# Kernel optimization log

Measured on AMD Instinct MI355X. Metric: run time of the kernel, lower is better.

## Reference

```python
import jax, jax.numpy as jnp
import numpy as np

N_POINTS = 500_000
NUM_SUPERNODES = 8192
MAX_DEGREE = 32
HIDDEN = 192
NDIM = 3
INPUT_DIM = 3
MAX_WAVELENGTH = 10000.0


def setup_inputs() -> dict:
    key = jax.random.key(0)
    k = jax.random.split(key, 8)
    rng = np.random.default_rng(0)
    # supernodes: unique node indices; each supernode gets MAX_DEGREE neighbor edges
    supernode_idx = np.sort(rng.choice(N_POINTS, size=NUM_SUPERNODES, replace=False))
    dst_idx = np.repeat(supernode_idx, MAX_DEGREE)              # [E] destination node ids
    src_idx = rng.integers(0, N_POINTS, size=NUM_SUPERNODES * MAX_DEGREE)  # [E] source node ids
    return {
        "input_feat": jax.random.normal(k[0], (N_POINTS, INPUT_DIM), dtype=jnp.float32),
        "input_pos": jax.random.uniform(k[1], (N_POINTS, NDIM), dtype=jnp.float32),
        "src_idx": jnp.asarray(src_idx, dtype=jnp.int64 if jax.config.jax_enable_x64 else jnp.int32),
        "dst_idx": jnp.asarray(dst_idx, dtype=jnp.int64 if jax.config.jax_enable_x64 else jnp.int32),
        "W_in": jax.random.normal(k[2], (INPUT_DIM, HIDDEN), dtype=jnp.float32) * 0.05,
        "b_in": jnp.zeros((HIDDEN,), dtype=jnp.float32),
        "W1": jax.random.normal(k[3], (2 * HIDDEN, HIDDEN), dtype=jnp.float32) * 0.05,
        "b1": jnp.zeros((HIDDEN,), dtype=jnp.float32),
        "W2": jax.random.normal(k[4], (HIDDEN, HIDDEN), dtype=jnp.float32) * 0.05,
        "b2": jnp.zeros((HIDDEN,), dtype=jnp.float32),
    }


def _sincos_embed(pos):
    # ContinuousSincosEmbed: HIDDEN split across NDIM axes, sin/cos halves each
    dim_per_axis = HIDDEN // NDIM  # 64 (even -> no padding)
    omega = 1.0 / MAX_WAVELENGTH ** (
        jnp.arange(0, dim_per_axis, 2, dtype=jnp.float32) / dim_per_axis
    )  # [32]
    ang = pos[:, :, None] * omega  # [N, NDIM, 32]
    emb = jnp.concatenate([jnp.sin(ang), jnp.cos(ang)], axis=-1)  # [N, NDIM, 64]
    return emb.reshape(pos.shape[0], HIDDEN)


def reference(input_feat, input_pos, src_idx, dst_idx, W_in, b_in, W1, b1, W2, b2):
    # node embedding: input projection + continuous sincos positional embed
    x = jnp.dot(input_feat, W_in) + b_in + _sincos_embed(input_pos)  # [N, H]
    # gather + concat edge features: [E, 2H]
    msg = jnp.concatenate([x[src_idx], x[dst_idx]], axis=1)
    # 2-layer message MLP (Linear-GELU-Linear)
    h = jax.nn.gelu(jnp.dot(msg, W1) + b1, approximate=False)
    h = jnp.dot(h, W2) + b2  # [E, H]
    # segment-mean over destination supernodes (fixed degree -> uniform counts)
    E = src_idx.shape[0]
    S = E // MAX_DEGREE
    seg = jnp.repeat(jnp.arange(S), MAX_DEGREE)
    pooled = jax.ops.segment_sum(h, seg, num_segments=S) / MAX_DEGREE  # [S, H]
    return pooled[None]  # [batch_size=1, S, H]
```

## Files before the change

kernel.cpp:

```cpp
#include <hip/hip_runtime.h>

#define DEG 32
#define SAW 232

typedef _Float16 half8 __attribute__((ext_vector_type(8)));
typedef __fp16 fp16x2 __attribute__((ext_vector_type(2)));
typedef float f32x4 __attribute__((ext_vector_type(4)));
typedef int int4v __attribute__((ext_vector_type(4)));

#define EXP2F(x)   __builtin_amdgcn_exp2f(x)
#define SIN_REV(x) __builtin_amdgcn_sinf(x)
#define COS_REV(x) __builtin_amdgcn_cosf(x)
#define RCPF(x)    __builtin_amdgcn_rcpf(x)
#define INV_2PI    0.15915494309189535f
#define TWO_LOG2E  2.8853900817779268f
#define NEG_L2_10K_O32 -0.41524101186092046f

__device__ __forceinline__ float gelu_f(float x){
  float z = 0.7978845608028654f * (x + 0.044715f * x * x * x);
  float e = EXP2F(TWO_LOG2E * z);
  float th = 1.0f - 2.0f * RCPF(1.0f + e);
  return 0.5f * x * (1.0f + th);
}

__device__ __forceinline__ int pkh(float a, float b){
  fp16x2 p = __builtin_amdgcn_cvt_pkrtz(a, b);
  return __builtin_bit_cast(int, p);
}

__device__ __forceinline__ void build_tile(_Float16 (*sA)[SAW], float (*sPos)[3],
    float* sOmg, const int* __restrict__ idx, int idx_stride, int base,
    const float* __restrict__ feat, const float* __restrict__ pos, int t){
  if (t < 32) sOmg[t] = EXP2F((float)t * NEG_L2_10K_O32) * INV_2PI;
  if (t < 64){
    int node = idx[(base + t) * idx_stride];
    sPos[t][0] = pos[3*node]; sPos[t][1] = pos[3*node+1]; sPos[t][2] = pos[3*node+2];
  }
  if (t >= 192){
    int e = t - 192;
    int node = idx[(base + e) * idx_stride];
    float f0 = feat[3*node], f1 = feat[3*node+1], f2 = feat[3*node+2];
    int4v v0; v0[0] = pkh(f0, f1); v0[1] = pkh(f2, 0.f); v0[2] = 0; v0[3] = 0;
    int4v z; z[0] = 0; z[1] = 0; z[2] = 0; z[3] = 0;
    *reinterpret_cast<int4v*>(&sA[e][192]) = v0;
    *reinterpret_cast<int4v*>(&sA[e][200]) = z;
    *reinterpret_cast<int4v*>(&sA[e][208]) = z;
    *reinterpret_cast<int4v*>(&sA[e][216]) = z;
  }
  __syncthreads();
  if (t < 192){
    int lane = t & 63, w = t >> 6;
    int r16 = lane & 15, g = lane >> 4;
    float om[8];
    #pragma unroll
    for (int j = 0; j < 8; j++) om[j] = sOmg[8*g + j];
    #pragma unroll
    for (int rr = 0; rr < 4; rr++){
      int row = r16 + rr*16;
      float p = sPos[row][w];
      float a[8];
      #pragma unroll
      for (int j = 0; j < 8; j++) a[j] = p * om[j];
      int4v sv, cv;
      #pragma unroll
      for (int j = 0; j < 4; j++){
        sv[j] = pkh(SIN_REV(a[2*j]), SIN_REV(a[2*j+1]));
        cv[j] = pkh(COS_REV(a[2*j]), COS_REV(a[2*j+1]));
      }
      int ch = w*8 + g;
      *reinterpret_cast<int4v*>(&sA[row][8*ch])     = sv;
      *reinterpret_cast<int4v*>(&sA[row][8*(ch+4)]) = cv;
    }
  }
  __syncthreads();
}

__device__ __forceinline__ void gemm_tile(f32x4 acc[4][3], const _Float16 (*sA)[SAW],
    const _Float16* __restrict__ Bt, int ln15, int grp, int wave){
  #pragma unroll
  for (int k6 = 0; k6 < 7; k6++){
    half8 Af[4];
    #pragma unroll
    for (int m = 0; m < 4; m++)
      Af[m] = *reinterpret_cast<const half8*>(&sA[m*16 + ln15][k6*32 + grp*8]);
    #pragma unroll
    for (int n = 0; n < 3; n++){
      half8 Bf = *reinterpret_cast<const half8*>(Bt + (wave*48 + n*16 + ln15)*224 + k6*32 + grp*8);
      #pragma unroll
      for (int m = 0; m < 4; m++)
        acc[m][n] = __builtin_amdgcn_mfma_f32_16x16x32_f16(Af[m], Bf, acc[m][n], 0, 0, 0);
    }
  }
}

__global__ void k0_prep(const float* __restrict__ W_in, const float* __restrict__ b_in,
    const float* __restrict__ W1, const float* __restrict__ b1,
    const float* __restrict__ W2,
    _Float16* __restrict__ w1tc, _Float16* __restrict__ w1bc,
    _Float16* __restrict__ w2t, float* __restrict__ bias_c){
  int id = blockIdx.x * 256 + threadIdx.x;
  if (id < 86016){
    int half_sel = id / 43008;
    int i = id - half_sel * 43008;
    int n = i / 224, k = i - n * 224;
    const float* Wh = W1 + half_sel * 192 * 192;
    _Float16* dst = half_sel ? w1bc : w1tc;
    if (k < 192) dst[i] = (_Float16)Wh[k*192 + n];
    else if (k < 195){
      int r = k - 192;
      float s = 0.f;
      for (int m = 0; m < 192; m++) s += W_in[r*192 + m] * Wh[m*192 + n];
      dst[i] = (_Float16)s;
    } else dst[i] = (_Float16)0.f;
  } else if (id < 122880){
    int i = id - 86016;
    int n = i / 192, k = i - n * 192;
    w2t[i] = (_Float16)(W2[k*192 + n] * 0.03125f);
  } else if (id < 123072){
    int n = id - 122880;
    float s = b1[n];
    for (int m = 0; m < 192; m++) s += b_in[m] * (W1[m*192 + n] + W1[(192+m)*192 + n]);
    bias_c[n] = s;
  }
}

__global__ __launch_bounds__(256) void k1_dst(const int* __restrict__ dst_idx,
    const float* __restrict__ feat, const float* __restrict__ pos,
    const _Float16* __restrict__ w1bc, const float* __restrict__ bias_c,
    _Float16* __restrict__ a_dst){
  __shared__ _Float16 sA[64][SAW];
  __shared__ float sPos[64][3];
  __shared__ float sOmg[32];
  int blk = blockIdx.x, t = threadIdx.x;
  build_tile(sA, sPos, sOmg, dst_idx, DEG, blk*64, feat, pos, t);
  int wave = t >> 6, lane = t & 63, ln15 = lane & 15, grp = lane >> 4;
  f32x4 acc[4][3];
  #pragma unroll
  for (int m = 0; m < 4; m++)
    #pragma unroll
    for (int n = 0; n < 3; n++) acc[m][n] = (f32x4){0.f, 0.f, 0.f, 0.f};
  gemm_tile(acc, sA, w1bc, ln15, grp, wave);
  #pragma unroll
  for (int n = 0; n < 3; n++){
    int col = wave*48 + n*16 + ln15;
    float bias = bias_c[col];
    #pragma unroll
    for (int m = 0; m < 4; m++)
      #pragma unroll
      for (int r = 0; r < 4; r++)
        a_dst[(blk*64 + m*16 + grp*4 + r)*192 + col] = (_Float16)(acc[m][n][r] + bias);
  }
}

__global__ __launch_bounds__(256) void k2_edge(const int* __restrict__ src_idx,
    const float* __restrict__ feat, const float* __restrict__ pos,
    const _Float16* __restrict__ w1tc, const _Float16* __restrict__ a_dst,
    _Float16* __restrict__ S1){
  __shared__ _Float16 sA[64][SAW];
  __shared__ float sPos[64][3];
  __shared__ float sOmg[32];
  int blk = blockIdx.x, t = threadIdx.x;
  build_tile(sA, sPos, sOmg, src_idx, 1, blk*64, feat, pos, t);
  int wave = t >> 6, lane = t & 63, ln15 = lane & 15, grp = lane >> 4;
  f32x4 acc[4][3];
  #pragma unroll
  for (int m = 0; m < 4; m++)
    #pragma unroll
    for (int n = 0; n < 3; n++) acc[m][n] = (f32x4){0.f, 0.f, 0.f, 0.f};
  gemm_tile(acc, sA, w1tc, ln15, grp, wave);
  const _Float16* adp = a_dst + blk*2*192;
  #pragma unroll
  for (int h = 0; h < 2; h++){
    #pragma unroll
    for (int n = 0; n < 3; n++){
      int col = wave*48 + n*16 + ln15;
      float ad = (float)adp[h*192 + col];
      float cs = 0.f;
      #pragma unroll
      for (int mm = 0; mm < 2; mm++){
        f32x4 a = acc[h*2 + mm][n];
        #pragma unroll
        for (int r = 0; r < 4; r++) cs += gelu_f(a[r] + ad);
      }
      cs += __shfl_xor(cs, 16, 64);
      cs += __shfl_xor(cs, 32, 64);
      if (grp == 0)
        S1[(blk*2 + h)*192 + col] = (_Float16)cs;
    }
  }
}

__global__ __launch_bounds__(256) void k3_out(const _Float16* __restrict__ S1,
    const _Float16* __restrict__ w2t, const float* __restrict__ b2,
    float* __restrict__ out){
  int blk = blockIdx.x, t = threadIdx.x;
  int wave = t >> 6, lane = t & 63, ln15 = lane & 15, grp = lane >> 4;
  f32x4 acc[4][3];
  #pragma unroll
  for (int m = 0; m < 4; m++)
    #pragma unroll
    for (int n = 0; n < 3; n++) acc[m][n] = (f32x4){0.f, 0.f, 0.f, 0.f};
  #pragma unroll
  for (int k6 = 0; k6 < 6; k6++){
    half8 Af[4];
    #pragma unroll
    for (int m = 0; m < 4; m++)
      Af[m] = *reinterpret_cast<const half8*>(S1 + (blk*64 + m*16 + ln15)*192 + k6*32 + grp*8);
    #pragma unroll
    for (int n = 0; n < 3; n++){
      half8 Bf = *reinterpret_cast<const half8*>(w2t + (wave*48 + n*16 + ln15)*192 + k6*32 + grp*8);
      #pragma unroll
      for (int m = 0; m < 4; m++)
        acc[m][n] = __builtin_amdgcn_mfma_f32_16x16x32_f16(Af[m], Bf, acc[m][n], 0, 0, 0);
    }
  }
  #pragma unroll
  for (int n = 0; n < 3; n++){
    int col = wave*48 + n*16 + ln15;
    float bias = b2[col];
    #pragma unroll
    for (int m = 0; m < 4; m++)
      #pragma unroll
      for (int r = 0; r < 4; r++)
        out[(blk*64 + m*16 + grp*4 + r)*192 + col] = acc[m][n][r] + bias;
  }
}

extern "C" void kernel_launch(void* const* d_in, const int* in_sizes, int n_in,
                              void* d_out, int out_size, void* d_ws, size_t ws_size,
                              hipStream_t stream) {
  const float* feat   = (const float*)d_in[0];
  const float* pos    = (const float*)d_in[1];
  const int*   src_i  = (const int*)  d_in[2];
  const int*   dst_i  = (const int*)  d_in[3];
  const float* W_in   = (const float*)d_in[4];
  const float* b_in   = (const float*)d_in[5];
  const float* W1     = (const float*)d_in[6];
  const float* b1     = (const float*)d_in[7];
  const float* W2     = (const float*)d_in[8];
  const float* b2     = (const float*)d_in[9];
  float* out = (float*)d_out;

  char* ws = (char*)d_ws;
  _Float16* w1tc   = (_Float16*)(ws);
  _Float16* w1bc   = (_Float16*)(ws + 86016);
  _Float16* w2t    = (_Float16*)(ws + 172032);
  float*    bias_c = (float*)   (ws + 245760);
  _Float16* a_dst  = (_Float16*)(ws + 246528);
  _Float16* S1     = (_Float16*)(ws + 3392256);

  k0_prep<<<481, 256, 0, stream>>>(W_in, b_in, W1, b1, W2, w1tc, w1bc, w2t, bias_c);
  k1_dst <<<128, 256, 0, stream>>>(dst_i, feat, pos, w1bc, bias_c, a_dst);
  k2_edge<<<4096, 256, 0, stream>>>(src_i, feat, pos, w1tc, a_dst, S1);
  k3_out <<<128, 256, 0, stream>>>(S1, w2t, b2, out);
}
```

Before: 152.7 us.

## Prefetch W1 fragments into registers, parallelize prep reductions, simplify GELU

The edge kernel now loads all of its W1 B-fragments into 21 half8 registers before the first barrier, so the global weight loads overlap the gather and trig phases instead of sitting inside the MFMA loop. The prep kernel replaces its serial 192-term dot products (folded bias and W_in·W1 columns) with wave-parallel reductions spread over more blocks. GELU is rewritten in an algebraically equivalent sigmoid form with fewer operations. The register prefetch raises VGPR pressure and may reduce occupancy in k2.

Result: no change. 152.3 us (-0.3%).

```diff
diff --git a/kernel.cpp b/kernel.cpp
--- a/kernel.cpp
+++ b/kernel.cpp
@@ -13,14 +13,14 @@
 #define COS_REV(x) __builtin_amdgcn_cosf(x)
 #define RCPF(x)    __builtin_amdgcn_rcpf(x)
 #define INV_2PI    0.15915494309189535f
-#define TWO_LOG2E  2.8853900817779268f
 #define NEG_L2_10K_O32 -0.41524101186092046f
 
 __device__ __forceinline__ float gelu_f(float x){
-  float z = 0.7978845608028654f * (x + 0.044715f * x * x * x);
-  float e = EXP2F(TWO_LOG2E * z);
-  float th = 1.0f - 2.0f * RCPF(1.0f + e);
-  return 0.5f * x * (1.0f + th);
+  float x2 = x * x;
+  float t  = __builtin_fmaf(0.10294824f, x2, 2.3022079f);
+  float e  = EXP2F(x * t);
+  float r  = RCPF(1.0f + e);
+  return __builtin_fmaf(-x, r, x);
 }
 
 __device__ __forceinline__ int pkh(float a, float b){
@@ -28,7 +28,13 @@
   return __builtin_bit_cast(int, p);
 }
 
-__device__ __forceinline__ void build_tile(_Float16 (*sA)[SAW], float (*sPos)[3],
+__device__ __forceinline__ float wave_reduce(float v){
+  #pragma unroll
+  for (int s = 1; s < 64; s <<= 1) v += __shfl_xor(v, s, 64);
+  return v;
+}
+
+__device__ __forceinline__ void tile_gather(_Float16 (*sA)[SAW], float (*sPos)[3],
     float* sOmg, const int* __restrict__ idx, int idx_stride, int base,
     const float* __restrict__ feat, const float* __restrict__ pos, int t){
   if (t < 32) sOmg[t] = EXP2F((float)t * NEG_L2_10K_O32) * INV_2PI;
@@ -47,7 +53,10 @@
     *reinterpret_cast<int4v*>(&sA[e][208]) = z;
     *reinterpret_cast<int4v*>(&sA[e][216]) = z;
   }
-  __syncthreads();
+}
+
+__device__ __forceinline__ void tile_trig(_Float16 (*sA)[SAW], const float (*sPos)[3],
+    const float* sOmg, int t){
   if (t < 192){
     int lane = t & 63, w = t >> 6;
     int r16 = lane & 15, g = lane >> 4;
@@ -72,7 +81,6 @@
       *reinterpret_cast<int4v*>(&sA[row][8*(ch+4)]) = cv;
     }
   }
-  __syncthreads();
 }
 
 __device__ __forceinline__ void gemm_tile(f32x4 acc[4][3], const _Float16 (*sA)[SAW],
@@ -105,22 +113,39 @@
     int n = i / 224, k = i - n * 224;
     const float* Wh = W1 + half_sel * 192 * 192;
     _Float16* dst = half_sel ? w1bc : w1tc;
-    if (k < 192) dst[i] = (_Float16)Wh[k*192 + n];
-    else if (k < 195){
-      int r = k - 192;
-      float s = 0.f;
-      for (int m = 0; m < 192; m++) s += W_in[r*192 + m] * Wh[m*192 + n];
-      dst[i] = (_Float16)s;
-    } else dst[i] = (_Float16)0.f;
+    if (k < 192)      dst[i] = (_Float16)Wh[k*192 + n];
+    else if (k >= 195) dst[i] = (_Float16)0.f;
   } else if (id < 122880){
     int i = id - 86016;
     int n = i / 192, k = i - n * 192;
     w2t[i] = (_Float16)(W2[k*192 + n] * 0.03125f);
-  } else if (id < 123072){
-    int n = id - 122880;
-    float s = b1[n];
-    for (int m = 0; m < 192; m++) s += b_in[m] * (W1[m*192 + n] + W1[(192+m)*192 + n]);
-    bias_c[n] = s;
+  } else if (id < 135168){
+    int o = (id - 122880) >> 6, lane = id & 63;
+    float s = 0.f;
+    #pragma unroll
+    for (int u = 0; u < 3; u++){
+      int m = lane + 64*u;
+      s += b_in[m] * (W1[m*192 + o] + W1[(m+192)*192 + o]);
+    }
+    s = wave_reduce(s);
+    if (lane == 0) bias_c[o] = s + b1[o];
+  } else if (id < 208896){
+    int o = (id - 135168) >> 6, lane = id & 63;
+    int half_sel = o / 576;
+    int rem = o - half_sel * 576;
+    int r = rem / 192, n = rem - r * 192;
+    const float* Wh = W1 + half_sel * 192 * 192;
+    float s = 0.f;
+    #pragma unroll
+    for (int u = 0; u < 3; u++){
+      int m = lane + 64*u;
+      s += W_in[r*192 + m] * Wh[m*192 + n];
+    }
+    s = wave_reduce(s);
+    if (lane == 0){
+      _Float16* dst = half_sel ? w1bc : w1tc;
+      dst[n*224 + 192 + r] = (_Float16)s;
+    }
   }
 }
 
@@ -132,7 +157,10 @@
   __shared__ float sPos[64][3];
   __shared__ float sOmg[32];
   int blk = blockIdx.x, t = threadIdx.x;
-  build_tile(sA, sPos, sOmg, dst_idx, DEG, blk*64, feat, pos, t);
+  tile_gather(sA, sPos, sOmg, dst_idx, DEG, blk*64, feat, pos, t);
+  __syncthreads();
+  tile_trig(sA, sPos, sOmg, t);
+  __syncthreads();
   int wave = t >> 6, lane = t & 63, ln15 = lane & 15, grp = lane >> 4;
   f32x4 acc[4][3];
   #pragma unroll
@@ -160,14 +188,40 @@
   __shared__ float sPos[64][3];
   __shared__ float sOmg[32];
   int blk = blockIdx.x, t = threadIdx.x;
-  build_tile(sA, sPos, sOmg, src_idx, 1, blk*64, feat, pos, t);
   int wave = t >> 6, lane = t & 63, ln15 = lane & 15, grp = lane >> 4;
+
+  tile_gather(sA, sPos, sOmg, src_idx, 1, blk*64, feat, pos, t);
+  half8 Breg[21];
+  {
+    const _Float16* bp = w1tc + (wave*48 + ln15)*224 + grp*8;
+    #pragma unroll
+    for (int n = 0; n < 3; n++)
+      #pragma unroll
+      for (int k6 = 0; k6 < 7; k6++)
+        Breg[n*7 + k6] = *reinterpret_cast<const half8*>(bp + n*16*224 + k6*32);
+  }
+  __syncthreads();
+  tile_trig(sA, sPos, sOmg, t);
+  __syncthreads();
+
   f32x4 acc[4][3];
   #pragma unroll
   for (int m = 0; m < 4; m++)
     #pragma unroll
     for (int n = 0; n < 3; n++) acc[m][n] = (f32x4){0.f, 0.f, 0.f, 0.f};
-  gemm_tile(acc, sA, w1tc, ln15, grp, wave);
+  #pragma unroll
+  for (int k6 = 0; k6 < 7; k6++){
+    half8 Af[4];
+    #pragma unroll
+    for (int m = 0; m < 4; m++)
+      Af[m] = *reinterpret_cast<const half8*>(&sA[m*16 + ln15][k6*32 + grp*8]);
+    #pragma unroll
+    for (int n = 0; n < 3; n++)
+      #pragma unroll
+      for (int m = 0; m < 4; m++)
+        acc[m][n] = __builtin_amdgcn_mfma_f32_16x16x32_f16(Af[m], Breg[n*7 + k6], acc[m][n], 0, 0, 0);
+  }
+
   const _Float16* adp = a_dst + blk*2*192;
   #pragma unroll
   for (int h = 0; h < 2; h++){
@@ -249,7 +303,7 @@
   _Float16* a_dst  = (_Float16*)(ws + 246528);
   _Float16* S1     = (_Float16*)(ws + 3392256);
 
-  k0_prep<<<481, 256, 0, stream>>>(W_in, b_in, W1, b1, W2, w1tc, w1bc, w2t, bias_c);
+  k0_prep<<<816, 256, 0, stream>>>(W_in, b_in, W1, b1, W2, w1tc, w1bc, w2t, bias_c);
   k1_dst <<<128, 256, 0, stream>>>(dst_i, feat, pos, w1bc, bias_c, a_dst);
   k2_edge<<<4096, 256, 0, stream>>>(src_i, feat, pos, w1tc, a_dst, S1);
   k3_out <<<128, 256, 0, stream>>>(S1, w2t, b2, out);
```
